# Optimization experiments

Measured on AMD Instinct MI355X. Metric: run time of the kernel, lower is better.

The kernel has to match this reference:

```python
import jax, jax.numpy as jnp
import numpy as np

S = 16384   # sequence length (tree derivation steps)
H = 512     # hidden size
E = 512     # action embedding size
R = 2048    # num_of_rules
L = 2       # GRU layers
PAD = -1    # learning_utils.PADDING_ACTION
OFF = 1     # learning_utils.UNIVERSAL_ACTION_OFFSET


def setup_inputs() -> dict:
    key = jax.random.key(0)
    ks = jax.random.split(key, 16)
    def n(k, shape, scale=0.05):
        return jax.random.normal(k, shape, jnp.float32) * scale
    emb = n(ks[1], (R + OFF, E)).at[PAD + OFF].set(0.0)  # padding_idx row zeroed
    return {
        "initial_state": n(ks[0], (L, 1, H)),
        "embedding": emb,
        "W_ih0": n(ks[2], (3 * H, 2 * E)),
        "W_hh0": n(ks[3], (3 * H, H)),
        "b_ih0": n(ks[4], (3 * H,)),
        "b_hh0": n(ks[5], (3 * H,)),
        "W_ih1": n(ks[6], (3 * H, H)),
        "W_hh1": n(ks[7], (3 * H, H)),
        "b_ih1": n(ks[8], (3 * H,)),
        "b_hh1": n(ks[9], (3 * H,)),
        "action_W": n(ks[10], (R, H)),
        "action_b": n(ks[11], (R,)),
        "value_W": n(ks[12], (1, H)),
        "value_b": n(ks[13], (1,)),
        "old_actions": jax.random.randint(ks[14], (S,), 0, R, jnp.int32),
        "old_parent_actions": jax.random.randint(ks[15], (S,), 0, R, jnp.int32),
    }


def gru_layer(x, h0, W_ih, W_hh, b_ih, b_hh):
    """Torch-semantics GRU over x:[S,In] with batch=1 squeezed; h0:[H]."""
    xi = x @ W_ih.T + b_ih  # precompute input gates [S, 3H]
    def step(h, xi_t):
        gh = h @ W_hh.T + b_hh
        xr, xz, xn = jnp.split(xi_t, 3)
        hr, hz, hn = jnp.split(gh, 3)
        r = jax.nn.sigmoid(xr + hr)
        z = jax.nn.sigmoid(xz + hz)
        nl = jnp.tanh(xn + r * hn)
        h_new = (1.0 - z) * nl + z * h
        return h_new, h_new
    _, out = jax.lax.scan(step, h0, xi)
    return out  # [S, H]


def reference(initial_state, embedding, W_ih0, W_hh0, b_ih0, b_hh0,
              W_ih1, W_hh1, b_ih1, b_hh1, action_W, action_b,
              value_W, value_b, old_actions, old_parent_actions):
    # teacher-forced shift: prepend PADDING_ACTION, drop last
    shifted = jnp.concatenate([jnp.array([PAD], old_actions.dtype), old_actions[:-1]])
    a_emb = embedding[shifted + OFF]             # [S, E]
    p_emb = embedding[old_parent_actions + OFF]  # [S, E]
    x = jnp.concatenate([a_emb, p_emb], axis=-1) # [S, 2E]
    h = gru_layer(x, initial_state[0, 0], W_ih0, W_hh0, b_ih0, b_hh0)
    out = gru_layer(h, initial_state[1, 0], W_ih1, W_hh1, b_ih1, b_hh1)
    log_probs = jax.nn.log_softmax(out @ action_W.T + action_b, axis=-1)  # [S, R]
    values = (out @ value_W.T + value_b)[:, 0]                            # [S]
    return log_probs, values
```

## Files before the change

kernel.cpp:

```cpp
#include <hip/hip_runtime.h>
#include <hip/hip_bf16.h>
#include <hip/hip_fp16.h>

typedef _Float16 f16;
typedef _Float16 f16x2 __attribute__((ext_vector_type(2)));
typedef _Float16 f16x4 __attribute__((ext_vector_type(4)));
typedef _Float16 f16x8 __attribute__((ext_vector_type(8)));
typedef float f32x4 __attribute__((ext_vector_type(4)));
typedef unsigned long long u64;

#define S_LEN 16384
#define NRULES 2048
#define CAP 2000000
#define FAST_TRIES 64

#define H1SEQ_OFF 0u
#define ACTW_OFF  (16u*1024*1024)
#define WIH0_OFF  (18u*1024*1024)
#define HB0F_OFF  (21u*1024*1024)
#define HB0S_OFF  (21u*1024*1024 + 4096)
#define HB1F_OFF  (21u*1024*1024 + 8192)
#define HB1S_OFF  (21u*1024*1024 + 12288)

#if __has_builtin(__builtin_amdgcn_rcpf)
#define RCPF(x) __builtin_amdgcn_rcpf(x)
#else
#define RCPF(x) (1.0f/(x))
#endif

union F2U { f16x2 f; unsigned u; };

__device__ __forceinline__ float sigf(float x){ return RCPF(1.0f + __expf(-x)); }
__device__ __forceinline__ float tanh_fast(float x){
  float ax = fabsf(x);
  float e = __expf(-2.0f*ax);
  float t = (1.0f - e) * RCPF(1.0f + e);
  return x >= 0.0f ? t : -t;
}
__device__ __forceinline__ float dot2(f16x2 a, f16x2 b, float c){
#if __has_builtin(__builtin_amdgcn_fdot2)
  return __builtin_amdgcn_fdot2(a, b, c, false);
#else
  return c + (float)a.x*(float)b.x + (float)a.y*(float)b.y;
#endif
}
__device__ __forceinline__ u64 aload64(const u64* p){
  return __hip_atomic_load(p, __ATOMIC_RELAXED, __HIP_MEMORY_SCOPE_AGENT);
}
__device__ __forceinline__ void apub64(u64* p, u64 v){
  (void)__hip_atomic_exchange(p, v, __ATOMIC_RELAXED, __HIP_MEMORY_SCOPE_AGENT);
}
__device__ __forceinline__ u64 load_sc0_u64(const u64* p){
  u64 v;
  asm volatile("global_load_dwordx2 %0, %1, off sc0\n\ts_waitcnt vmcnt(0)"
               : "=v"(v) : "v"(p) : "memory");
  return v;
}
__device__ __forceinline__ void store_u64(u64* p, u64 v){
  asm volatile("global_store_dwordx2 %0, %1, off"
               :: "v"(p), "v"(v) : "memory");
}

__global__ __launch_bounds__(256) void gather_x(
    const float* __restrict__ emb, const int* __restrict__ act,
    const int* __restrict__ par, f16* __restrict__ X)
{
  const int t = blockIdx.x, lid = threadIdx.x;
  const int ia = (t == 0) ? 0 : (act[t-1] + 1);
  const int ip = par[t] + 1;
  const int half = lid >> 7;
  const int k = (lid & 127) << 2;
  const float* src = emb + (size_t)(half ? ip : ia) * 512 + k;
  float4 v = *(const float4*)src;
  f16x4 o; o.x=(f16)v.x; o.y=(f16)v.y; o.z=(f16)v.z; o.w=(f16)v.w;
  *(f16x4*)&X[(size_t)t*1024 + (half<<9) + k] = o;
}

__global__ __launch_bounds__(256) void cvt_k(const float* __restrict__ in,
                                             f16* __restrict__ out, int n)
{
  const int i = (blockIdx.x*256 + threadIdx.x) << 2;
  if (i >= n) return;
  float4 v = *(const float4*)&in[i];
  f16x4 o; o.x=(f16)v.x; o.y=(f16)v.y; o.z=(f16)v.z; o.w=(f16)v.w;
  *(f16x4*)&out[i] = o;
}

__global__ __launch_bounds__(256) void init_ctrl(const float* __restrict__ init, char* ws)
{
  const int lid = threadIdx.x;
  u64* f0 = (u64*)(ws + HB0F_OFF);
  u64* s0 = (u64*)(ws + HB0S_OFF);
  u64* f1 = (u64*)(ws + HB1F_OFF);
  u64* s1 = (u64*)(ws + HB1S_OFF);
  F2U a; a.f.x=(f16)init[2*lid];     a.f.y=(f16)init[2*lid+1];
  F2U c; c.f.x=(f16)init[512+2*lid]; c.f.y=(f16)init[512+2*lid+1];
  const u64 inval = (u64)0xF0000000u << 32;
  const u64 sa = (u64)a.u, sc = (u64)c.u;
  f0[lid] = inval; f0[256+lid] = sa;
  s0[lid] = inval; s0[256+lid] = sa;
  f1[lid] = inval; f1[256+lid] = sc;
  s1[lid] = inval; s1[256+lid] = sc;
}

template<typename OutT>
__global__ __launch_bounds__(256) void gemm_f16(
    const f16* __restrict__ A, const f16* __restrict__ B,
    const float* __restrict__ bias, OutT* __restrict__ C,
    int M, int N, int K)
{
  __shared__ __align__(16) f16 At[4][128][8];
  __shared__ __align__(16) f16 Bt[4][128][8];
  const int lid = threadIdx.x;
  const int mtiles = M >> 7;
  const int bm = blockIdx.x % mtiles;
  const int bn = blockIdx.x / mtiles;
  const int m0 = bm << 7, n0 = bn << 7;
  const int lane = lid & 63, w = lid >> 6;
  const int wm = (w >> 1) << 6, wn = (w & 1) << 6;
  f32x4 acc[4][4] = {};
  const int nk = K >> 5;
  const int row1 = lid >> 2, j1 = lid & 3;
  for (int kt = 0; kt < nk; ++kt){
    const int kb = kt << 5;
    *(f16x8*)&At[j1][row1][0]    = *(const f16x8*)&A[(size_t)(m0+row1)*K    + kb + j1*8];
    *(f16x8*)&At[j1][row1+64][0] = *(const f16x8*)&A[(size_t)(m0+row1+64)*K + kb + j1*8];
    *(f16x8*)&Bt[j1][row1][0]    = *(const f16x8*)&B[(size_t)(n0+row1)*K    + kb + j1*8];
    *(f16x8*)&Bt[j1][row1+64][0] = *(const f16x8*)&B[(size_t)(n0+row1+64)*K + kb + j1*8];
    __syncthreads();
    const int kc = lane >> 4, rr = lane & 15;
    f16x8 aF[4], bF[4];
    #pragma unroll
    for (int m=0;m<4;m++) aF[m] = *(const f16x8*)&At[kc][wm + m*16 + rr][0];
    #pragma unroll
    for (int n=0;n<4;n++) bF[n] = *(const f16x8*)&Bt[kc][wn + n*16 + rr][0];
    #pragma unroll
    for (int m=0;m<4;m++)
      #pragma unroll
      for (int n=0;n<4;n++)
        acc[m][n] = __builtin_amdgcn_mfma_f32_16x16x32_f16(aF[m], bF[n], acc[m][n], 0,0,0);
    __syncthreads();
  }
  const int rr = lane & 15, rg = lane >> 4;
  #pragma unroll
  for (int n=0;n<4;n++){
    const int gcol = n0 + wn + n*16 + rr;
    const float bv = bias[gcol];
    #pragma unroll
    for (int m=0;m<4;m++){
      #pragma unroll
      for (int r=0;r<4;r++){
        const int grow = m0 + wm + m*16 + rg*4 + r;
        C[(size_t)grow*N + gcol] = (OutT)(acc[m][n][r] + bv);
      }
    }
  }
}

__global__ __launch_bounds__(256, 1) void scan_rings(
    const float* __restrict__ Whh0, const float* __restrict__ bhh0,
    const float* __restrict__ Wih1, const float* __restrict__ bih1,
    const float* __restrict__ Whh1, const float* __restrict__ bhh1,
    const float* __restrict__ init, const f16* __restrict__ xi0,
    u64* __restrict__ h0seq, char* ws)
{
  const int lid = threadIdx.x;
  const int bid = blockIdx.x;
  f16x2* h1seq = (f16x2*)(ws + H1SEQ_OFF);
  u64* hb0f = (u64*)(ws + HB0F_OFF);
  u64* hb0s = (u64*)(ws + HB0S_OFF);
  u64* hb1f = (u64*)(ws + HB1F_OFF);
  u64* hb1s = (u64*)(ws + HB1S_OFF);
  __shared__ f16x2 hx[256];
  __shared__ f16x2 hh[256];

  const int lane7 = bid & 7, grp = bid >> 3;
  bool fast_ok = true;

  if (lane7 == 0 && grp < 8){
    const int b = grp;
    const int ksub = lid & 3, row = (b << 6) + (lid >> 2);
    const bool owner = (ksub == 0);
    f16x2 wr[64], wz[64], wn[64];
    #pragma unroll
    for (int i=0;i<64;i++){
      const int k0 = (ksub + (i<<2)) << 1;
      float2 a = *(const float2*)&Whh0[(size_t)row*512         + k0];
      float2 bb= *(const float2*)&Whh0[(size_t)(512+row)*512   + k0];
      float2 c = *(const float2*)&Whh0[(size_t)(1024+row)*512  + k0];
      wr[i].x=(f16)a.x;  wr[i].y=(f16)a.y;
      wz[i].x=(f16)bb.x; wz[i].y=(f16)bb.y;
      wn[i].x=(f16)c.x;  wn[i].y=(f16)c.y;
    }
    float bhr=0.f, bhz=0.f, bhn=0.f;
    if (owner){ bhr=bhh0[row]; bhz=bhh0[512+row]; bhn=bhh0[1024+row]; }

    for (int q=0; q<S_LEN; ++q){
      float xr=0.f, xz=0.f, xn=0.f;
      if (owner){
        const f16* xp = xi0 + (size_t)q*1536;
        xr=(float)xp[row]; xz=(float)xp[512+row]; xn=(float)xp[1024+row];
      }
      {
        const int par = (q+1)&1;
        const u64* pf = hb0f + par*256 + lid;
        const u64* ps = hb0s + par*256 + lid;
        u64 cell = 0; bool got = false;
        if (fast_ok){
          for (int k=0;k<FAST_TRIES;k++){
            u64 v = load_sc0_u64(pf);
            if ((unsigned)(v>>32) == (unsigned)q){ cell=v; got=true; break; }
          }
          if (!got) fast_ok = false;
        }
        if (!got){
          int it=0;
          for(;;){ u64 v = aload64(ps);
                   if ((unsigned)(v>>32) == (unsigned)q){ cell=v; break; }
                   if (++it > CAP){ cell=v; break; } }
        }
        F2U cu; cu.u = (unsigned)cell; hx[lid] = cu.f;
      }
      __syncthreads();
      float ar=0.f, az=0.f, an=0.f;
      #pragma unroll
      for (int i=0;i<64;i++){
        f16x2 hv = hx[ksub + (i<<2)];
        ar = dot2(wr[i], hv, ar); az = dot2(wz[i], hv, az); an = dot2(wn[i], hv, an);
      }
      ar += __shfl_xor(ar,1); ar += __shfl_xor(ar,2);
      az += __shfl_xor(az,1); az += __shfl_xor(az,2);
      an += __shfl_xor(an,1); an += __shfl_xor(an,2);
      float hnew = 0.f;
      if (owner){
        float r  = sigf(xr + ar + bhr);
        float z  = sigf(xz + az + bhz);
        float nl = tanh_fast(xn + r*(an + bhn));
        hnew = (1.0f - z)*nl + z*(float)hx[row>>1][row&1];
      }
      float hp = __shfl(hnew, (lid & 192) + ((lid+4) & 63));
      if ((lid & 7) == 0){
        F2U pr; pr.f.x=(f16)hnew; pr.f.y=(f16)hp;
        const int j = (b<<5) + (lid>>3);
        const u64 tagged = ((u64)(unsigned)(q+1)<<32) | (u64)pr.u;
        store_u64(&hb0f[(q&1)*256 + j], tagged);
        apub64(&hb0s[(q&1)*256 + j], tagged);
        apub64(&h0seq[(size_t)q*256 + j], tagged);
      }
      __syncthreads();
    }
  } else if (lane7 == 1 && grp < 16){
    const int u = grp;
    const int ksub = lid & 7, row = (u << 5) + (lid >> 3);
    const bool owner = (ksub == 0);
    f16x2 ur[32], uz[32], un[32], vr[32], vz[32], vn[32];
    #pragma unroll
    for (int i=0;i<32;i++){
      const int k0 = (ksub + (i<<3)) << 1;
      float2 a = *(const float2*)&Wih1[(size_t)row*512        + k0];
      float2 bb= *(const float2*)&Wih1[(size_t)(512+row)*512  + k0];
      float2 c = *(const float2*)&Wih1[(size_t)(1024+row)*512 + k0];
      float2 d = *(const float2*)&Whh1[(size_t)row*512        + k0];
      float2 e = *(const float2*)&Whh1[(size_t)(512+row)*512  + k0];
      float2 f = *(const float2*)&Whh1[(size_t)(1024+row)*512 + k0];
      ur[i].x=(f16)a.x;  ur[i].y=(f16)a.y;
      uz[i].x=(f16)bb.x; uz[i].y=(f16)bb.y;
      un[i].x=(f16)c.x;  un[i].y=(f16)c.y;
      vr[i].x=(f16)d.x;  vr[i].y=(f16)d.y;
      vz[i].x=(f16)e.x;  vz[i].y=(f16)e.y;
      vn[i].x=(f16)f.x;  vn[i].y=(f16)f.y;
    }
    float bir=0.f,biz=0.f,bin=0.f, bhr=0.f,bhz=0.f,bhn=0.f;
    if (owner){
      bir=bih1[row]; biz=bih1[512+row]; bin=bih1[1024+row];
      bhr=bhh1[row]; bhz=bhh1[512+row]; bhn=bhh1[1024+row];
    }

    u64 ca_pref = 0;
    for (int t=0; t<S_LEN; ++t){
      const u64* pa = h0seq + (size_t)t*256 + lid;
      const int par = (t+1)&1;
      const u64* pf = hb1f + par*256 + lid;
      const u64* ps = hb1s + par*256 + lid;
      u64 ca=0, cb=0; bool ga=false, gb=false;
      if ((unsigned)(ca_pref>>32) == (unsigned)(t+1)){ ca=ca_pref; ga=true; }
      if (fast_ok){
        for (int k=0; k<FAST_TRIES && !(ga&&gb); ++k){
          if(!ga){ u64 v=aload64(pa);
                   if((unsigned)(v>>32)==(unsigned)(t+1)){ca=v;ga=true;} }
          if(!gb){ u64 v=load_sc0_u64(pf);
                   if((unsigned)(v>>32)==(unsigned)t){cb=v;gb=true;} }
        }
        if (!gb) fast_ok = false;
      }
      if (!(ga&&gb)){
        int it=0;
        while(!(ga&&gb)){
          if(!ga){ u64 v=aload64(pa);
                   if((unsigned)(v>>32)==(unsigned)(t+1)){ca=v;ga=true;} }
          if(!gb){ u64 v=aload64(ps);
                   if((unsigned)(v>>32)==(unsigned)t){cb=v;gb=true;} }
          if (++it > CAP) break;
        }
      }
      F2U xa; xa.u = (unsigned)ca; hx[lid] = xa.f;
      F2U hc; hc.u = (unsigned)cb; hh[lid] = hc.f;
      __syncthreads();
      if (t+1 < S_LEN) ca_pref = aload64(pa + 256);
      float ir=0.f, iz=0.f, in_=0.f, hr=0.f, hz=0.f, hn=0.f;
      #pragma unroll
      for (int i=0;i<32;i++){
        f16x2 xv = hx[ksub + (i<<3)];
        f16x2 hv = hh[ksub + (i<<3)];
        ir = dot2(ur[i], xv, ir); iz = dot2(uz[i], xv, iz); in_ = dot2(un[i], xv, in_);
        hr = dot2(vr[i], hv, hr); hz = dot2(vz[i], hv, hz); hn  = dot2(vn[i], hv, hn);
      }
      #pragma unroll
      for (int d=1; d<8; d<<=1){
        ir += __shfl_xor(ir,d); iz += __shfl_xor(iz,d); in_ += __shfl_xor(in_,d);
        hr += __shfl_xor(hr,d); hz += __shfl_xor(hz,d); hn  += __shfl_xor(hn,d);
      }
      float hnew = 0.f;
      if (owner){
        float r  = sigf(ir + bir + hr + bhr);
        float z  = sigf(iz + biz + hz + bhz);
        float nl = tanh_fast(in_ + bin + r*(hn + bhn));
        hnew = (1.0f - z)*nl + z*(float)hh[row>>1][row&1];
      }
      float hp = __shfl(hnew, (lid & 192) + ((lid+8) & 63));
      if ((lid & 15) == 0){
        F2U pr; pr.f.x=(f16)hnew; pr.f.y=(f16)hp;
        const int j = (u<<4) + (lid>>4);
        const u64 tagged = ((u64)(unsigned)(t+1)<<32) | (u64)pr.u;
        store_u64(&hb1f[(t&1)*256 + j], tagged);
        apub64(&hb1s[(t&1)*256 + j], tagged);
        h1seq[(size_t)t*256 + j] = pr.f;
      }
      __syncthreads();
    }
  }
}

__global__ __launch_bounds__(256) void logsoftmax_k(float* __restrict__ lp)
{
  const int t = blockIdx.x, lid = threadIdx.x;
  float* row = lp + (size_t)t*2048;
  float4 a = ((const float4*)row)[lid*2];
  float4 b = ((const float4*)row)[lid*2+1];
  float m = fmaxf(fmaxf(fmaxf(a.x,a.y),fmaxf(a.z,a.w)),
                  fmaxf(fmaxf(b.x,b.y),fmaxf(b.z,b.w)));
  #pragma unroll
  for (int off=1; off<64; off<<=1) m = fmaxf(m, __shfl_xor(m, off));
  __shared__ float redm[4], reds[4];
  const int lane = lid & 63, wvi = lid >> 6;
  if (lane==0) redm[wvi] = m;
  __syncthreads();
  m = fmaxf(fmaxf(redm[0],redm[1]), fmaxf(redm[2],redm[3]));
  float s = __expf(a.x-m)+__expf(a.y-m)+__expf(a.z-m)+__expf(a.w-m)
          + __expf(b.x-m)+__expf(b.y-m)+__expf(b.z-m)+__expf(b.w-m);
  #pragma unroll
  for (int off=1; off<64; off<<=1) s += __shfl_xor(s, off);
  if (lane==0) reds[wvi] = s;
  __syncthreads();
  s = reds[0]+reds[1]+reds[2]+reds[3];
  const float lg = m + __logf(s);
  a.x-=lg; a.y-=lg; a.z-=lg; a.w-=lg;
  b.x-=lg; b.y-=lg; b.z-=lg; b.w-=lg;
  ((float4*)row)[lid*2]   = a;
  ((float4*)row)[lid*2+1] = b;
}

__global__ __launch_bounds__(256) void values_k(
    const f16* __restrict__ h1, const float* __restrict__ vW,
    const float* __restrict__ vb, float* __restrict__ outv, int S)
{
  const int gt = (int)((blockIdx.x*256 + threadIdx.x) >> 6);
  if (gt >= S) return;
  const int lane = threadIdx.x & 63;
  const f16* rowp = h1 + (size_t)gt*512;
  float s = 0.f;
  #pragma unroll
  for (int j=0;j<8;j++){
    const int k = lane + (j<<6);
    s += (float)rowp[k] * vW[k];
  }
  #pragma unroll
  for (int off=32; off; off>>=1) s += __shfl_down(s, off);
  if (lane==0) outv[gt] = s + vb[0];
}

extern "C" void kernel_launch(void* const* d_in, const int* in_sizes, int n_in,
                              void* d_out, int out_size, void* d_ws, size_t ws_size,
                              hipStream_t stream) {
  const float* init = (const float*)d_in[0];
  const float* emb  = (const float*)d_in[1];
  const float* Wih0 = (const float*)d_in[2];
  const float* Whh0 = (const float*)d_in[3];
  const float* bih0 = (const float*)d_in[4];
  const float* bhh0 = (const float*)d_in[5];
  const float* Wih1 = (const float*)d_in[6];
  const float* Whh1 = (const float*)d_in[7];
  const float* bih1 = (const float*)d_in[8];
  const float* bhh1 = (const float*)d_in[9];
  const float* actW = (const float*)d_in[10];
  const float* actb = (const float*)d_in[11];
  const float* valW = (const float*)d_in[12];
  const float* valb = (const float*)d_in[13];
  const int*   acts = (const int*)d_in[14];
  const int*   pars = (const int*)d_in[15];
  float* out = (float*)d_out;
  char*  w   = (char*)d_ws;

  f16* h1seq = (f16*)(w + H1SEQ_OFF);
  f16* actWh = (f16*)(w + ACTW_OFF);
  f16* Wih0h = (f16*)(w + WIH0_OFF);
  f16* xi0   = (f16*)d_out;
  f16* X     = (f16*)((char*)d_out + 48u*1024*1024);
  u64* h0seq = (u64*)((char*)d_out + 80u*1024*1024);

  hipMemsetAsync(h0seq, 0, (size_t)S_LEN*256*8, stream);
  gather_x<<<S_LEN, 256, 0, stream>>>(emb, acts, pars, X);
  cvt_k<<<1536, 256, 0, stream>>>(Wih0, Wih0h, 1536*1024);
  cvt_k<<<1024, 256, 0, stream>>>(actW, actWh, 2048*512);
  init_ctrl<<<1, 256, 0, stream>>>(init, w);

  gemm_f16<f16><<<128*12, 256, 0, stream>>>(X, Wih0h, bih0, xi0, S_LEN, 1536, 1024);

  scan_rings<<<128, 256, 0, stream>>>(Whh0, bhh0, Wih1, bih1, Whh1, bhh1,
                                      init, xi0, h0seq, w);

  gemm_f16<float><<<128*16, 256, 0, stream>>>(h1seq, actWh, actb, out, S_LEN, NRULES, 512);
  logsoftmax_k<<<S_LEN, 256, 0, stream>>>(out);
  values_k<<<S_LEN/4, 256, 0, stream>>>(h1seq, valW, valb, out + (size_t)S_LEN*NRULES, S_LEN);
}
```

Before: 30.43 ms.

## Add dedicated publisher wavefront to scan blocks, decoupling global stores from compute waves

Each scan block gets a fifth wavefront that takes over publishing the new hidden state to the global ring buffers and sequence arrays. Compute waves now write hnew into shared memory and meet the publisher at lightweight barriers that wait only on LDS counters, which replaces the cross-lane shuffle pairing. The goal is to take global store and atomic latency off the compute waves' per-step critical path. The cost is one more wave per block and an extra shared-memory hop, and publication can still become a serialisation point.

Result: slower. 31.65 ms (+4.0%).

```diff
diff --git a/kernel.cpp b/kernel.cpp
--- a/kernel.cpp
+++ b/kernel.cpp
@@ -60,6 +60,7 @@
   asm volatile("global_store_dwordx2 %0, %1, off"
                :: "v"(p), "v"(v) : "memory");
 }
+#define BAR_LGKM() asm volatile("s_waitcnt lgkmcnt(0)\n\ts_barrier" ::: "memory")
 
 __global__ __launch_bounds__(256) void gather_x(
     const float* __restrict__ emb, const int* __restrict__ act,
@@ -157,7 +158,7 @@
   }
 }
 
-__global__ __launch_bounds__(256, 1) void scan_rings(
+__global__ __launch_bounds__(320, 1) void scan_rings(
     const float* __restrict__ Whh0, const float* __restrict__ bhh0,
     const float* __restrict__ Wih1, const float* __restrict__ bih1,
     const float* __restrict__ Whh1, const float* __restrict__ bhh1,
@@ -173,170 +174,184 @@
   u64* hb1s = (u64*)(ws + HB1S_OFF);
   __shared__ f16x2 hx[256];
   __shared__ f16x2 hh[256];
+  __shared__ float hnb[64];
 
   const int lane7 = bid & 7, grp = bid >> 3;
   bool fast_ok = true;
 
   if (lane7 == 0 && grp < 8){
     const int b = grp;
-    const int ksub = lid & 3, row = (b << 6) + (lid >> 2);
-    const bool owner = (ksub == 0);
-    f16x2 wr[64], wz[64], wn[64];
-    #pragma unroll
-    for (int i=0;i<64;i++){
-      const int k0 = (ksub + (i<<2)) << 1;
-      float2 a = *(const float2*)&Whh0[(size_t)row*512         + k0];
-      float2 bb= *(const float2*)&Whh0[(size_t)(512+row)*512   + k0];
-      float2 c = *(const float2*)&Whh0[(size_t)(1024+row)*512  + k0];
-      wr[i].x=(f16)a.x;  wr[i].y=(f16)a.y;
-      wz[i].x=(f16)bb.x; wz[i].y=(f16)bb.y;
-      wn[i].x=(f16)c.x;  wn[i].y=(f16)c.y;
-    }
-    float bhr=0.f, bhz=0.f, bhn=0.f;
-    if (owner){ bhr=bhh0[row]; bhz=bhh0[512+row]; bhn=bhh0[1024+row]; }
-
-    for (int q=0; q<S_LEN; ++q){
-      float xr=0.f, xz=0.f, xn=0.f;
-      if (owner){
-        const f16* xp = xi0 + (size_t)q*1536;
-        xr=(float)xp[row]; xz=(float)xp[512+row]; xn=(float)xp[1024+row];
-      }
-      {
-        const int par = (q+1)&1;
-        const u64* pf = hb0f + par*256 + lid;
-        const u64* ps = hb0s + par*256 + lid;
-        u64 cell = 0; bool got = false;
-        if (fast_ok){
-          for (int k=0;k<FAST_TRIES;k++){
-            u64 v = load_sc0_u64(pf);
-            if ((unsigned)(v>>32) == (unsigned)q){ cell=v; got=true; break; }
-          }
-          if (!got) fast_ok = false;
-        }
-        if (!got){
-          int it=0;
-          for(;;){ u64 v = aload64(ps);
-                   if ((unsigned)(v>>32) == (unsigned)q){ cell=v; break; }
-                   if (++it > CAP){ cell=v; break; } }
-        }
-        F2U cu; cu.u = (unsigned)cell; hx[lid] = cu.f;
-      }
-      __syncthreads();
-      float ar=0.f, az=0.f, an=0.f;
+    if (lid < 256){
+      const int ksub = lid & 3, row = (b << 6) + (lid >> 2);
+      const bool owner = (ksub == 0);
+      f16x2 wr[64], wz[64], wn[64];
       #pragma unroll
       for (int i=0;i<64;i++){
-        f16x2 hv = hx[ksub + (i<<2)];
-        ar = dot2(wr[i], hv, ar); az = dot2(wz[i], hv, az); an = dot2(wn[i], hv, an);
-      }
-      ar += __shfl_xor(ar,1); ar += __shfl_xor(ar,2);
-      az += __shfl_xor(az,1); az += __shfl_xor(az,2);
-      an += __shfl_xor(an,1); an += __shfl_xor(an,2);
-      float hnew = 0.f;
-      if (owner){
-        float r  = sigf(xr + ar + bhr);
-        float z  = sigf(xz + az + bhz);
-        float nl = tanh_fast(xn + r*(an + bhn));
-        hnew = (1.0f - z)*nl + z*(float)hx[row>>1][row&1];
-      }
-      float hp = __shfl(hnew, (lid & 192) + ((lid+4) & 63));
-      if ((lid & 7) == 0){
-        F2U pr; pr.f.x=(f16)hnew; pr.f.y=(f16)hp;
-        const int j = (b<<5) + (lid>>3);
-        const u64 tagged = ((u64)(unsigned)(q+1)<<32) | (u64)pr.u;
-        store_u64(&hb0f[(q&1)*256 + j], tagged);
-        apub64(&hb0s[(q&1)*256 + j], tagged);
-        apub64(&h0seq[(size_t)q*256 + j], tagged);
-      }
-      __syncthreads();
+        const int k0 = (ksub + (i<<2)) << 1;
+        float2 a = *(const float2*)&Whh0[(size_t)row*512         + k0];
+        float2 bb= *(const float2*)&Whh0[(size_t)(512+row)*512   + k0];
+        float2 c = *(const float2*)&Whh0[(size_t)(1024+row)*512  + k0];
+        wr[i].x=(f16)a.x;  wr[i].y=(f16)a.y;
+        wz[i].x=(f16)bb.x; wz[i].y=(f16)bb.y;
+        wn[i].x=(f16)c.x;  wn[i].y=(f16)c.y;
+      }
+      float bhr=0.f, bhz=0.f, bhn=0.f;
+      if (owner){ bhr=bhh0[row]; bhz=bhh0[512+row]; bhn=bhh0[1024+row]; }
+
+      for (int q=0; q<S_LEN; ++q){
+        float xr=0.f, xz=0.f, xn=0.f;
+        if (owner){
+          const f16* xp = xi0 + (size_t)q*1536;
+          xr=(float)xp[row]; xz=(float)xp[512+row]; xn=(float)xp[1024+row];
+        }
+        {
+          const int par = (q+1)&1;
+          const u64* pf = hb0f + par*256 + lid;
+          const u64* ps = hb0s + par*256 + lid;
+          u64 cell = 0; bool got = false;
+          if (fast_ok){
+            for (int k=0;k<FAST_TRIES;k++){
+              u64 v = load_sc0_u64(pf);
+              if ((unsigned)(v>>32) == (unsigned)q){ cell=v; got=true; break; }
+            }
+            if (!got) fast_ok = false;
+          }
+          if (!got){
+            int it=0;
+            for(;;){ u64 v = aload64(ps);
+                     if ((unsigned)(v>>32) == (unsigned)q){ cell=v; break; }
+                     if (++it > CAP){ cell=v; break; } }
+          }
+          F2U cu; cu.u = (unsigned)cell; hx[lid] = cu.f;
+        }
+        BAR_LGKM();
+        float ar=0.f, az=0.f, an=0.f;
+        #pragma unroll
+        for (int i=0;i<64;i++){
+          f16x2 hv = hx[ksub + (i<<2)];
+          ar = dot2(wr[i], hv, ar); az = dot2(wz[i], hv, az); an = dot2(wn[i], hv, an);
+        }
+        ar += __shfl_xor(ar,1); ar += __shfl_xor(ar,2);
+        az += __shfl_xor(az,1); az += __shfl_xor(az,2);
+        an += __shfl_xor(an,1); an += __shfl_xor(an,2);
+        if (owner){
+          float r  = sigf(xr + ar + bhr);
+          float z  = sigf(xz + az + bhz);
+          float nl = tanh_fast(xn + r*(an + bhn));
+          float hnew = (1.0f - z)*nl + z*(float)hx[row>>1][row&1];
+          hnb[lid>>2] = hnew;
+        }
+        BAR_LGKM();
+      }
+    } else {
+      const int pl = lid - 256;
+      for (int q=0; q<S_LEN; ++q){
+        BAR_LGKM();
+        BAR_LGKM();
+        if (pl < 32){
+          F2U pr; pr.f.x=(f16)hnb[2*pl]; pr.f.y=(f16)hnb[2*pl+1];
+          const int j = (b<<5) + pl;
+          const u64 tagged = ((u64)(unsigned)(q+1)<<32) | (u64)pr.u;
+          store_u64(&hb0f[(q&1)*256 + j], tagged);
+          apub64(&hb0s[(q&1)*256 + j], tagged);
+          apub64(&h0seq[(size_t)q*256 + j], tagged);
+        }
+      }
     }
   } else if (lane7 == 1 && grp < 16){
     const int u = grp;
-    const int ksub = lid & 7, row = (u << 5) + (lid >> 3);
-    const bool owner = (ksub == 0);
-    f16x2 ur[32], uz[32], un[32], vr[32], vz[32], vn[32];
-    #pragma unroll
-    for (int i=0;i<32;i++){
-      const int k0 = (ksub + (i<<3)) << 1;
-      float2 a = *(const float2*)&Wih1[(size_t)row*512        + k0];
-      float2 bb= *(const float2*)&Wih1[(size_t)(512+row)*512  + k0];
-      float2 c = *(const float2*)&Wih1[(size_t)(1024+row)*512 + k0];
-      float2 d = *(const float2*)&Whh1[(size_t)row*512        + k0];
-      float2 e = *(const float2*)&Whh1[(size_t)(512+row)*512  + k0];
-      float2 f = *(const float2*)&Whh1[(size_t)(1024+row)*512 + k0];
-      ur[i].x=(f16)a.x;  ur[i].y=(f16)a.y;
-      uz[i].x=(f16)bb.x; uz[i].y=(f16)bb.y;
-      un[i].x=(f16)c.x;  un[i].y=(f16)c.y;
-      vr[i].x=(f16)d.x;  vr[i].y=(f16)d.y;
-      vz[i].x=(f16)e.x;  vz[i].y=(f16)e.y;
-      vn[i].x=(f16)f.x;  vn[i].y=(f16)f.y;
-    }
-    float bir=0.f,biz=0.f,bin=0.f, bhr=0.f,bhz=0.f,bhn=0.f;
-    if (owner){
-      bir=bih1[row]; biz=bih1[512+row]; bin=bih1[1024+row];
-      bhr=bhh1[row]; bhz=bhh1[512+row]; bhn=bhh1[1024+row];
-    }
-
-    u64 ca_pref = 0;
-    for (int t=0; t<S_LEN; ++t){
-      const u64* pa = h0seq + (size_t)t*256 + lid;
-      const int par = (t+1)&1;
-      const u64* pf = hb1f + par*256 + lid;
-      const u64* ps = hb1s + par*256 + lid;
-      u64 ca=0, cb=0; bool ga=false, gb=false;
-      if ((unsigned)(ca_pref>>32) == (unsigned)(t+1)){ ca=ca_pref; ga=true; }
-      if (fast_ok){
-        for (int k=0; k<FAST_TRIES && !(ga&&gb); ++k){
-          if(!ga){ u64 v=aload64(pa);
-                   if((unsigned)(v>>32)==(unsigned)(t+1)){ca=v;ga=true;} }
-          if(!gb){ u64 v=load_sc0_u64(pf);
-                   if((unsigned)(v>>32)==(unsigned)t){cb=v;gb=true;} }
-        }
-        if (!gb) fast_ok = false;
-      }
-      if (!(ga&&gb)){
-        int it=0;
-        while(!(ga&&gb)){
-          if(!ga){ u64 v=aload64(pa);
-                   if((unsigned)(v>>32)==(unsigned)(t+1)){ca=v;ga=true;} }
-          if(!gb){ u64 v=aload64(ps);
-                   if((unsigned)(v>>32)==(unsigned)t){cb=v;gb=true;} }
-          if (++it > CAP) break;
-        }
-      }
-      F2U xa; xa.u = (unsigned)ca; hx[lid] = xa.f;
-      F2U hc; hc.u = (unsigned)cb; hh[lid] = hc.f;
-      __syncthreads();
-      if (t+1 < S_LEN) ca_pref = aload64(pa + 256);
-      float ir=0.f, iz=0.f, in_=0.f, hr=0.f, hz=0.f, hn=0.f;
+    if (lid < 256){
+      const int ksub = lid & 7, row = (u << 5) + (lid >> 3);
+      const bool owner = (ksub == 0);
+      f16x2 ur[32], uz[32], un[32], vr[32], vz[32], vn[32];
       #pragma unroll
       for (int i=0;i<32;i++){
-        f16x2 xv = hx[ksub + (i<<3)];
-        f16x2 hv = hh[ksub + (i<<3)];
-        ir = dot2(ur[i], xv, ir); iz = dot2(uz[i], xv, iz); in_ = dot2(un[i], xv, in_);
-        hr = dot2(vr[i], hv, hr); hz = dot2(vz[i], hv, hz); hn  = dot2(vn[i], hv, hn);
-      }
-      #pragma unroll
-      for (int d=1; d<8; d<<=1){
-        ir += __shfl_xor(ir,d); iz += __shfl_xor(iz,d); in_ += __shfl_xor(in_,d);
-        hr += __shfl_xor(hr,d); hz += __shfl_xor(hz,d); hn  += __shfl_xor(hn,d);
-      }
-      float hnew = 0.f;
+        const int k0 = (ksub + (i<<3)) << 1;
+        float2 a = *(const float2*)&Wih1[(size_t)row*512        + k0];
+        float2 bb= *(const float2*)&Wih1[(size_t)(512+row)*512  + k0];
+        float2 c = *(const float2*)&Wih1[(size_t)(1024+row)*512 + k0];
+        float2 d = *(const float2*)&Whh1[(size_t)row*512        + k0];
+        float2 e = *(const float2*)&Whh1[(size_t)(512+row)*512  + k0];
+        float2 f = *(const float2*)&Whh1[(size_t)(1024+row)*512 + k0];
+        ur[i].x=(f16)a.x;  ur[i].y=(f16)a.y;
+        uz[i].x=(f16)bb.x; uz[i].y=(f16)bb.y;
+        un[i].x=(f16)c.x;  un[i].y=(f16)c.y;
+        vr[i].x=(f16)d.x;  vr[i].y=(f16)d.y;
+        vz[i].x=(f16)e.x;  vz[i].y=(f16)e.y;
+        vn[i].x=(f16)f.x;  vn[i].y=(f16)f.y;
+      }
+      float bir=0.f,biz=0.f,bin=0.f, bhr=0.f,bhz=0.f,bhn=0.f;
       if (owner){
-        float r  = sigf(ir + bir + hr + bhr);
-        float z  = sigf(iz + biz + hz + bhz);
-        float nl = tanh_fast(in_ + bin + r*(hn + bhn));
-        hnew = (1.0f - z)*nl + z*(float)hh[row>>1][row&1];
-      }
-      float hp = __shfl(hnew, (lid & 192) + ((lid+8) & 63));
-      if ((lid & 15) == 0){
-        F2U pr; pr.f.x=(f16)hnew; pr.f.y=(f16)hp;
-        const int j = (u<<4) + (lid>>4);
-        const u64 tagged = ((u64)(unsigned)(t+1)<<32) | (u64)pr.u;
-        store_u64(&hb1f[(t&1)*256 + j], tagged);
-        apub64(&hb1s[(t&1)*256 + j], tagged);
-        h1seq[(size_t)t*256 + j] = pr.f;
-      }
-      __syncthreads();
+        bir=bih1[row]; biz=bih1[512+row]; bin=bih1[1024+row];
+        bhr=bhh1[row]; bhz=bhh1[512+row]; bhn=bhh1[1024+row];
+      }
+
+      for (int t=0; t<S_LEN; ++t){
+        {
+          const u64* pa = h0seq + (size_t)t*256 + lid;
+          const int par = (t+1)&1;
+          const u64* pf = hb1f + par*256 + lid;
+          const u64* ps = hb1s + par*256 + lid;
+          u64 ca=0, cb=0; bool ga=false, gb=false;
+          if (fast_ok){
+            for (int k=0; k<FAST_TRIES && !(ga&&gb); ++k){
+              if(!ga){ u64 v=aload64(pa);
+                       if((unsigned)(v>>32)==(unsigned)(t+1)){ca=v;ga=true;} }
+              if(!gb){ u64 v=load_sc0_u64(pf);
+                       if((unsigned)(v>>32)==(unsigned)t){cb=v;gb=true;} }
+            }
+            if (!gb) fast_ok = false;
+          }
+          if (!(ga&&gb)){
+            int it=0;
+            while(!(ga&&gb)){
+              if(!ga){ u64 v=aload64(pa);
+                       if((unsigned)(v>>32)==(unsigned)(t+1)){ca=v;ga=true;} }
+              if(!gb){ u64 v=aload64(ps);
+                       if((unsigned)(v>>32)==(unsigned)t){cb=v;gb=true;} }
+              if (++it > CAP) break;
+            }
+          }
+          F2U xa; xa.u = (unsigned)ca; hx[lid] = xa.f;
+          F2U hc; hc.u = (unsigned)cb; hh[lid] = hc.f;
+        }
+        BAR_LGKM();
+        float ir=0.f, iz=0.f, in_=0.f, hr=0.f, hz=0.f, hn=0.f;
+        #pragma unroll
+        for (int i=0;i<32;i++){
+          f16x2 xv = hx[ksub + (i<<3)];
+          f16x2 hv = hh[ksub + (i<<3)];
+          ir = dot2(ur[i], xv, ir); iz = dot2(uz[i], xv, iz); in_ = dot2(un[i], xv, in_);
+          hr = dot2(vr[i], hv, hr); hz = dot2(vz[i], hv, hz); hn  = dot2(vn[i], hv, hn);
+        }
+        #pragma unroll
+        for (int d=1; d<8; d<<=1){
+          ir += __shfl_xor(ir,d); iz += __shfl_xor(iz,d); in_ += __shfl_xor(in_,d);
+          hr += __shfl_xor(hr,d); hz += __shfl_xor(hz,d); hn  += __shfl_xor(hn,d);
+        }
+        if (owner){
+          float r  = sigf(ir + bir + hr + bhr);
+          float z  = sigf(iz + biz + hz + bhz);
+          float nl = tanh_fast(in_ + bin + r*(hn + bhn));
+          float hnew = (1.0f - z)*nl + z*(float)hh[row>>1][row&1];
+          hnb[lid>>3] = hnew;
+        }
+        BAR_LGKM();
+      }
+    } else {
+      const int pl = lid - 256;
+      for (int t=0; t<S_LEN; ++t){
+        BAR_LGKM();
+        BAR_LGKM();
+        if (pl < 16){
+          F2U pr; pr.f.x=(f16)hnb[2*pl]; pr.f.y=(f16)hnb[2*pl+1];
+          const int j = (u<<4) + pl;
+          const u64 tagged = ((u64)(unsigned)(t+1)<<32) | (u64)pr.u;
+          store_u64(&hb1f[(t&1)*256 + j], tagged);
+          apub64(&hb1s[(t&1)*256 + j], tagged);
+          h1seq[(size_t)t*256 + j] = pr.f;
+        }
+      }
     }
   }
 }
@@ -426,7 +441,7 @@
 
   gemm_f16<f16><<<128*12, 256, 0, stream>>>(X, Wih0h, bih0, xi0, S_LEN, 1536, 1024);
 
-  scan_rings<<<128, 256, 0, stream>>>(Whh0, bhh0, Wih1, bih1, Whh1, bhh1,
+  scan_rings<<<128, 320, 0, stream>>>(Whh0, bhh0, Wih1, bih1, Whh1, bhh1,
                                       init, xi0, h0seq, w);
 
   gemm_f16<float><<<128*16, 256, 0, stream>>>(h1seq, actWh, actb, out, S_LEN, NRULES, 512);
```

## Co-locate both GRU layers per workgroup and pass layer-0 state through shared memory

Applied to the files above, without the earlier changes.

Replaces the separate layer-0 and layer-1 ring workgroups with 16 workgroups of 768 threads. Each one holds a 32-row slice of layer 0 and a 32-row slice of layer 1, with layer 1 running one step behind layer 0 inside the same loop. Layer-0 output reaches layer 1 through LDS instead of a global h0seq buffer, and cross-workgroup exchange still goes through tagged flag rings. This removes the h0seq memset, the global staging and polling between layers, and prefetches the next step's input gates. The cost is spreading layer-0 rows over 16 blocks instead of 8, which means more participants in each cross-block sync. Barriers now use s_waitcnt lgkmcnt plus s_barrier.

New measurement: 53.70 ms. 1.76x slower.

```diff
diff --git a/kernel.cpp b/kernel.cpp
--- a/kernel.cpp
+++ b/kernel.cpp
@@ -60,6 +60,7 @@
   asm volatile("global_store_dwordx2 %0, %1, off"
                :: "v"(p), "v"(v) : "memory");
 }
+#define BAR_LGKM() asm volatile("s_waitcnt lgkmcnt(0)\n\ts_barrier" ::: "memory")
 
 __global__ __launch_bounds__(256) void gather_x(
     const float* __restrict__ emb, const int* __restrict__ act,
@@ -86,21 +87,18 @@
   *(f16x4*)&out[i] = o;
 }
 
-__global__ __launch_bounds__(256) void init_ctrl(const float* __restrict__ init, char* ws)
+__global__ __launch_bounds__(256) void init_ctrl(char* ws)
 {
   const int lid = threadIdx.x;
-  u64* f0 = (u64*)(ws + HB0F_OFF);
-  u64* s0 = (u64*)(ws + HB0S_OFF);
-  u64* f1 = (u64*)(ws + HB1F_OFF);
-  u64* s1 = (u64*)(ws + HB1S_OFF);
-  F2U a; a.f.x=(f16)init[2*lid];     a.f.y=(f16)init[2*lid+1];
-  F2U c; c.f.x=(f16)init[512+2*lid]; c.f.y=(f16)init[512+2*lid+1];
   const u64 inval = (u64)0xF0000000u << 32;
-  const u64 sa = (u64)a.u, sc = (u64)c.u;
-  f0[lid] = inval; f0[256+lid] = sa;
-  s0[lid] = inval; s0[256+lid] = sa;
-  f1[lid] = inval; f1[256+lid] = sc;
-  s1[lid] = inval; s1[256+lid] = sc;
+  u64* F0 = (u64*)(ws + HB0F_OFF);
+  u64* S0 = (u64*)(ws + HB0S_OFF);
+  u64* F1 = (u64*)(ws + HB1F_OFF);
+  u64* S1 = (u64*)(ws + HB1S_OFF);
+  F0[lid]=inval; F0[256+lid]=inval;
+  S0[lid]=inval; S0[256+lid]=inval;
+  F1[lid]=inval; F1[256+lid]=inval;
+  S1[lid]=inval; S1[256+lid]=inval;
 }
 
 template<typename OutT>
@@ -157,186 +155,186 @@
   }
 }
 
-__global__ __launch_bounds__(256, 1) void scan_rings(
+__global__ __launch_bounds__(768, 1) void scan_m(
     const float* __restrict__ Whh0, const float* __restrict__ bhh0,
     const float* __restrict__ Wih1, const float* __restrict__ bih1,
     const float* __restrict__ Whh1, const float* __restrict__ bhh1,
     const float* __restrict__ init, const f16* __restrict__ xi0,
-    u64* __restrict__ h0seq, char* ws)
-{
-  const int lid = threadIdx.x;
-  const int bid = blockIdx.x;
+    char* ws)
+{
+  const int lid = threadIdx.x, bid = blockIdx.x;
+  if (bid & 7) return;
+  const int grp = bid >> 3;
   f16x2* h1seq = (f16x2*)(ws + H1SEQ_OFF);
-  u64* hb0f = (u64*)(ws + HB0F_OFF);
-  u64* hb0s = (u64*)(ws + HB0S_OFF);
-  u64* hb1f = (u64*)(ws + HB1F_OFF);
-  u64* hb1s = (u64*)(ws + HB1S_OFF);
-  __shared__ f16x2 hx[256];
-  __shared__ f16x2 hh[256];
-
-  const int lane7 = bid & 7, grp = bid >> 3;
+  u64* F0 = (u64*)(ws + HB0F_OFF);
+  u64* S0 = (u64*)(ws + HB0S_OFF);
+  u64* F1 = (u64*)(ws + HB1F_OFF);
+  u64* S1 = (u64*)(ws + HB1S_OFF);
+  __shared__ f16x2 hb[2][512];
   bool fast_ok = true;
 
-  if (lane7 == 0 && grp < 8){
-    const int b = grp;
-    const int ksub = lid & 3, row = (b << 6) + (lid >> 2);
+  if (lid < 256){
+    const int ksub = lid & 7, r = lid >> 3, row = (grp << 5) + r;
     const bool owner = (ksub == 0);
-    f16x2 wr[64], wz[64], wn[64];
-    #pragma unroll
-    for (int i=0;i<64;i++){
-      const int k0 = (ksub + (i<<2)) << 1;
-      float2 a = *(const float2*)&Whh0[(size_t)row*512         + k0];
-      float2 bb= *(const float2*)&Whh0[(size_t)(512+row)*512   + k0];
-      float2 c = *(const float2*)&Whh0[(size_t)(1024+row)*512  + k0];
-      wr[i].x=(f16)a.x;  wr[i].y=(f16)a.y;
-      wz[i].x=(f16)bb.x; wz[i].y=(f16)bb.y;
-      wn[i].x=(f16)c.x;  wn[i].y=(f16)c.y;
-    }
-    float bhr=0.f, bhz=0.f, bhn=0.f;
-    if (owner){ bhr=bhh0[row]; bhz=bhh0[512+row]; bhn=bhh0[1024+row]; }
-
-    for (int q=0; q<S_LEN; ++q){
-      float xr=0.f, xz=0.f, xn=0.f;
-      if (owner){
-        const f16* xp = xi0 + (size_t)q*1536;
-        xr=(float)xp[row]; xz=(float)xp[512+row]; xn=(float)xp[1024+row];
-      }
-      {
-        const int par = (q+1)&1;
-        const u64* pf = hb0f + par*256 + lid;
-        const u64* ps = hb0s + par*256 + lid;
-        u64 cell = 0; bool got = false;
-        if (fast_ok){
-          for (int k=0;k<FAST_TRIES;k++){
-            u64 v = load_sc0_u64(pf);
-            if ((unsigned)(v>>32) == (unsigned)q){ cell=v; got=true; break; }
-          }
-          if (!got) fast_ok = false;
-        }
-        if (!got){
-          int it=0;
-          for(;;){ u64 v = aload64(ps);
-                   if ((unsigned)(v>>32) == (unsigned)q){ cell=v; break; }
-                   if (++it > CAP){ cell=v; break; } }
-        }
-        F2U cu; cu.u = (unsigned)cell; hx[lid] = cu.f;
-      }
-      __syncthreads();
-      float ar=0.f, az=0.f, an=0.f;
-      #pragma unroll
-      for (int i=0;i<64;i++){
-        f16x2 hv = hx[ksub + (i<<2)];
-        ar = dot2(wr[i], hv, ar); az = dot2(wz[i], hv, az); an = dot2(wn[i], hv, an);
-      }
-      ar += __shfl_xor(ar,1); ar += __shfl_xor(ar,2);
-      az += __shfl_xor(az,1); az += __shfl_xor(az,2);
-      an += __shfl_xor(an,1); an += __shfl_xor(an,2);
-      float hnew = 0.f;
-      if (owner){
-        float r  = sigf(xr + ar + bhr);
-        float z  = sigf(xz + az + bhz);
-        float nl = tanh_fast(xn + r*(an + bhn));
-        hnew = (1.0f - z)*nl + z*(float)hx[row>>1][row&1];
-      }
-      float hp = __shfl(hnew, (lid & 192) + ((lid+4) & 63));
-      if ((lid & 7) == 0){
-        F2U pr; pr.f.x=(f16)hnew; pr.f.y=(f16)hp;
-        const int j = (b<<5) + (lid>>3);
-        const u64 tagged = ((u64)(unsigned)(q+1)<<32) | (u64)pr.u;
-        store_u64(&hb0f[(q&1)*256 + j], tagged);
-        apub64(&hb0s[(q&1)*256 + j], tagged);
-        apub64(&h0seq[(size_t)q*256 + j], tagged);
-      }
-      __syncthreads();
-    }
-  } else if (lane7 == 1 && grp < 16){
-    const int u = grp;
-    const int ksub = lid & 7, row = (u << 5) + (lid >> 3);
-    const bool owner = (ksub == 0);
-    f16x2 ur[32], uz[32], un[32], vr[32], vz[32], vn[32];
+    f16x2 wr[32], wz[32], wn[32];
     #pragma unroll
     for (int i=0;i<32;i++){
       const int k0 = (ksub + (i<<3)) << 1;
-      float2 a = *(const float2*)&Wih1[(size_t)row*512        + k0];
-      float2 bb= *(const float2*)&Wih1[(size_t)(512+row)*512  + k0];
-      float2 c = *(const float2*)&Wih1[(size_t)(1024+row)*512 + k0];
-      float2 d = *(const float2*)&Whh1[(size_t)row*512        + k0];
-      float2 e = *(const float2*)&Whh1[(size_t)(512+row)*512  + k0];
-      float2 f = *(const float2*)&Whh1[(size_t)(1024+row)*512 + k0];
-      ur[i].x=(f16)a.x;  ur[i].y=(f16)a.y;
-      uz[i].x=(f16)bb.x; uz[i].y=(f16)bb.y;
-      un[i].x=(f16)c.x;  un[i].y=(f16)c.y;
-      vr[i].x=(f16)d.x;  vr[i].y=(f16)d.y;
-      vz[i].x=(f16)e.x;  vz[i].y=(f16)e.y;
-      vn[i].x=(f16)f.x;  vn[i].y=(f16)f.y;
+      float2 a = *(const float2*)&Whh0[(size_t)row*512         + k0];
+      float2 b = *(const float2*)&Whh0[(size_t)(512+row)*512   + k0];
+      float2 c = *(const float2*)&Whh0[(size_t)(1024+row)*512  + k0];
+      wr[i].x=(f16)a.x; wr[i].y=(f16)a.y;
+      wz[i].x=(f16)b.x; wz[i].y=(f16)b.y;
+      wn[i].x=(f16)c.x; wn[i].y=(f16)c.y;
+    }
+    float bhr=0.f,bhz=0.f,bhn=0.f, xr=0.f,xz=0.f,xn=0.f, pxr=0.f,pxz=0.f,pxn=0.f;
+    if (owner){
+      bhr=bhh0[row]; bhz=bhh0[512+row]; bhn=bhh0[1024+row];
+      xr=(float)xi0[row]; xz=(float)xi0[512+row]; xn=(float)xi0[1024+row];
+    }
+    { F2U s; s.f.x=(f16)init[2*lid]; s.f.y=(f16)init[2*lid+1]; hb[0][lid]=s.f; }
+    BAR_LGKM();
+
+    for (int q=0; q<=S_LEN; ++q){
+      const int p = (q+1)&1;
+      if (q < S_LEN){
+        if (owner && q+1 < S_LEN){
+          const f16* xp = xi0 + (size_t)(q+1)*1536;
+          pxr=(float)xp[row]; pxz=(float)xp[512+row]; pxn=(float)xp[1024+row];
+        }
+        const f16x2* cur = hb[q&1];
+        float ar=0.f, az=0.f, an=0.f;
+        #pragma unroll
+        for (int i=0;i<32;i++){
+          f16x2 hv = cur[ksub + (i<<3)];
+          ar = dot2(wr[i],hv,ar); az = dot2(wz[i],hv,az); an = dot2(wn[i],hv,an);
+        }
+        ar += __shfl_xor(ar,1); ar += __shfl_xor(ar,2); ar += __shfl_xor(ar,4);
+        az += __shfl_xor(az,1); az += __shfl_xor(az,2); az += __shfl_xor(az,4);
+        an += __shfl_xor(an,1); an += __shfl_xor(an,2); an += __shfl_xor(an,4);
+        float hnew = 0.f;
+        if (owner){
+          float r_ = sigf(xr + ar + bhr);
+          float z_ = sigf(xz + az + bhz);
+          float nl = tanh_fast(xn + r_*(an + bhn));
+          hnew = (1.0f - z_)*nl + z_*(float)cur[row>>1][row&1];
+          xr=pxr; xz=pxz; xn=pxn;
+        }
+        float hp = __shfl(hnew, ((lid&63)+8)&63);
+        if ((lid & 15) == 0){
+          F2U pr; pr.f.x=(f16)hnew; pr.f.y=(f16)hp;
+          const int j = (grp<<4) + (lid>>4);
+          const u64 tg = ((u64)(unsigned)(q+1)<<32) | (u64)pr.u;
+          store_u64(&F0[p*256 + j], tg);
+          apub64(&S0[p*256 + j], tg);
+        }
+        {
+          const u64* pf = F0 + p*256 + lid;
+          const u64* ps = S0 + p*256 + lid;
+          u64 cell=0; bool got=false;
+          if (fast_ok){
+            for (int k=0;k<FAST_TRIES;k++){
+              u64 v = load_sc0_u64(pf);
+              if ((unsigned)(v>>32) == (unsigned)(q+1)){ cell=v; got=true; break; }
+            }
+            if (!got) fast_ok = false;
+          }
+          if (!got){
+            int it=0;
+            for(;;){ u64 v = aload64(ps);
+                     if ((unsigned)(v>>32) == (unsigned)(q+1)){ cell=v; break; }
+                     if (++it > CAP){ cell=v; break; } }
+          }
+          F2U cu; cu.u = (unsigned)cell; hb[p][lid] = cu.f;
+        }
+      }
+      BAR_LGKM();
+    }
+  } else {
+    const int local = lid - 256;
+    const int ksub16 = local & 15, ksubh = ksub16 & 7;
+    const int r = local >> 4, row = (grp << 5) + r;
+    const bool grpA = (ksub16 < 8);
+    const bool owner = (ksub16 == 0);
+    const float* Wsel = grpA ? Wih1 : Whh1;
+    const int base = grpA ? 0 : 256;
+    f16x2 wa[32], wb[32], wc[32];
+    #pragma unroll
+    for (int i=0;i<32;i++){
+      const int k0 = (ksubh + (i<<3)) << 1;
+      float2 a = *(const float2*)&Wsel[(size_t)row*512         + k0];
+      float2 b = *(const float2*)&Wsel[(size_t)(512+row)*512   + k0];
+      float2 c = *(const float2*)&Wsel[(size_t)(1024+row)*512  + k0];
+      wa[i].x=(f16)a.x; wa[i].y=(f16)a.y;
+      wb[i].x=(f16)b.x; wb[i].y=(f16)b.y;
+      wc[i].x=(f16)c.x; wc[i].y=(f16)c.y;
     }
     float bir=0.f,biz=0.f,bin=0.f, bhr=0.f,bhz=0.f,bhn=0.f;
     if (owner){
       bir=bih1[row]; biz=bih1[512+row]; bin=bih1[1024+row];
       bhr=bhh1[row]; bhz=bhh1[512+row]; bhn=bhh1[1024+row];
     }
-
-    u64 ca_pref = 0;
-    for (int t=0; t<S_LEN; ++t){
-      const u64* pa = h0seq + (size_t)t*256 + lid;
-      const int par = (t+1)&1;
-      const u64* pf = hb1f + par*256 + lid;
-      const u64* ps = hb1s + par*256 + lid;
-      u64 ca=0, cb=0; bool ga=false, gb=false;
-      if ((unsigned)(ca_pref>>32) == (unsigned)(t+1)){ ca=ca_pref; ga=true; }
-      if (fast_ok){
-        for (int k=0; k<FAST_TRIES && !(ga&&gb); ++k){
-          if(!ga){ u64 v=aload64(pa);
-                   if((unsigned)(v>>32)==(unsigned)(t+1)){ca=v;ga=true;} }
-          if(!gb){ u64 v=load_sc0_u64(pf);
-                   if((unsigned)(v>>32)==(unsigned)t){cb=v;gb=true;} }
-        }
-        if (!gb) fast_ok = false;
+    if (local < 256){
+      F2U s; s.f.x=(f16)init[512+2*local]; s.f.y=(f16)init[512+2*local+1];
+      hb[0][256+local] = s.f;
+    }
+    BAR_LGKM();
+
+    for (int q=0; q<=S_LEN; ++q){
+      const int p = (q+1)&1;
+      if (q >= 1){
+        const f16x2* cur = hb[q&1];
+        float sa=0.f, sb=0.f, sc=0.f;
+        #pragma unroll
+        for (int i=0;i<32;i++){
+          f16x2 hv = cur[base + ksubh + (i<<3)];
+          sa = dot2(wa[i],hv,sa); sb = dot2(wb[i],hv,sb); sc = dot2(wc[i],hv,sc);
+        }
+        sa += __shfl_xor(sa,1); sa += __shfl_xor(sa,2); sa += __shfl_xor(sa,4);
+        sb += __shfl_xor(sb,1); sb += __shfl_xor(sb,2); sb += __shfl_xor(sb,4);
+        sc += __shfl_xor(sc,1); sc += __shfl_xor(sc,2); sc += __shfl_xor(sc,4);
+        float oa = __shfl_xor(sa,8), ob = __shfl_xor(sb,8), oc = __shfl_xor(sc,8);
+        float hnew = 0.f;
+        if (owner){
+          float r_ = sigf(sa + bir + oa + bhr);
+          float z_ = sigf(sb + biz + ob + bhz);
+          float nl = tanh_fast(sc + bin + r_*(oc + bhn));
+          hnew = (1.0f - z_)*nl + z_*(float)cur[256 + (row>>1)][row&1];
+        }
+        float hp = __shfl(hnew, ((lid&63)+16)&63);
+        if ((local & 31) == 0){
+          F2U pr; pr.f.x=(f16)hnew; pr.f.y=(f16)hp;
+          const int j = (grp<<4) + (local>>5);
+          h1seq[(size_t)(q-1)*256 + j] = pr.f;
+          if (q < S_LEN){
+            const u64 tg = ((u64)(unsigned)(q+1)<<32) | (u64)pr.u;
+            store_u64(&F1[p*256 + j], tg);
+            apub64(&S1[p*256 + j], tg);
+          }
+        }
       }
-      if (!(ga&&gb)){
-        int it=0;
-        while(!(ga&&gb)){
-          if(!ga){ u64 v=aload64(pa);
-                   if((unsigned)(v>>32)==(unsigned)(t+1)){ca=v;ga=true;} }
-          if(!gb){ u64 v=aload64(ps);
-                   if((unsigned)(v>>32)==(unsigned)t){cb=v;gb=true;} }
-          if (++it > CAP) break;
-        }
+      if (q == 0){
+        if (local < 256) hb[1][256+local] = hb[0][256+local];
+      } else if (q < S_LEN && local < 256){
+        const u64* pf = F1 + p*256 + local;
+        const u64* ps = S1 + p*256 + local;
+        u64 cell=0; bool got=false;
+        if (fast_ok){
+          for (int k=0;k<FAST_TRIES;k++){
+            u64 v = load_sc0_u64(pf);
+            if ((unsigned)(v>>32) == (unsigned)(q+1)){ cell=v; got=true; break; }
+          }
+          if (!got) fast_ok = false;
+        }
+        if (!got){
+          int it=0;
+          for(;;){ u64 v = aload64(ps);
+                   if ((unsigned)(v>>32) == (unsigned)(q+1)){ cell=v; break; }
+                   if (++it > CAP){ cell=v; break; } }
+        }
+        F2U cu; cu.u = (unsigned)cell; hb[p][256+local] = cu.f;
       }
-      F2U xa; xa.u = (unsigned)ca; hx[lid] = xa.f;
-      F2U hc; hc.u = (unsigned)cb; hh[lid] = hc.f;
-      __syncthreads();
-      if (t+1 < S_LEN) ca_pref = aload64(pa + 256);
-      float ir=0.f, iz=0.f, in_=0.f, hr=0.f, hz=0.f, hn=0.f;
-      #pragma unroll
-      for (int i=0;i<32;i++){
-        f16x2 xv = hx[ksub + (i<<3)];
-        f16x2 hv = hh[ksub + (i<<3)];
-        ir = dot2(ur[i], xv, ir); iz = dot2(uz[i], xv, iz); in_ = dot2(un[i], xv, in_);
-        hr = dot2(vr[i], hv, hr); hz = dot2(vz[i], hv, hz); hn  = dot2(vn[i], hv, hn);
-      }
-      #pragma unroll
-      for (int d=1; d<8; d<<=1){
-        ir += __shfl_xor(ir,d); iz += __shfl_xor(iz,d); in_ += __shfl_xor(in_,d);
-        hr += __shfl_xor(hr,d); hz += __shfl_xor(hz,d); hn  += __shfl_xor(hn,d);
-      }
-      float hnew = 0.f;
-      if (owner){
-        float r  = sigf(ir + bir + hr + bhr);
-        float z  = sigf(iz + biz + hz + bhz);
-        float nl = tanh_fast(in_ + bin + r*(hn + bhn));
-        hnew = (1.0f - z)*nl + z*(float)hh[row>>1][row&1];
-      }
-      float hp = __shfl(hnew, (lid & 192) + ((lid+8) & 63));
-      if ((lid & 15) == 0){
-        F2U pr; pr.f.x=(f16)hnew; pr.f.y=(f16)hp;
-        const int j = (u<<4) + (lid>>4);
-        const u64 tagged = ((u64)(unsigned)(t+1)<<32) | (u64)pr.u;
-        store_u64(&hb1f[(t&1)*256 + j], tagged);
-        apub64(&hb1s[(t&1)*256 + j], tagged);
-        h1seq[(size_t)t*256 + j] = pr.f;
-      }
-      __syncthreads();
+      BAR_LGKM();
     }
   }
 }
@@ -414,20 +412,18 @@
   f16* h1seq = (f16*)(w + H1SEQ_OFF);
   f16* actWh = (f16*)(w + ACTW_OFF);
   f16* Wih0h = (f16*)(w + WIH0_OFF);
-  f16* xi0   = (f16*)d_out;
-  f16* X     = (f16*)((char*)d_out + 48u*1024*1024);
-  u64* h0seq = (u64*)((char*)d_out + 80u*1024*1024);
-
-  hipMemsetAsync(h0seq, 0, (size_t)S_LEN*256*8, stream);
+  f16* xi0 = (f16*)d_out;
+  f16* X   = (f16*)((char*)d_out + 48u*1024*1024);
+
   gather_x<<<S_LEN, 256, 0, stream>>>(emb, acts, pars, X);
   cvt_k<<<1536, 256, 0, stream>>>(Wih0, Wih0h, 1536*1024);
   cvt_k<<<1024, 256, 0, stream>>>(actW, actWh, 2048*512);
-  init_ctrl<<<1, 256, 0, stream>>>(init, w);
+  init_ctrl<<<1, 256, 0, stream>>>(w);
 
   gemm_f16<f16><<<128*12, 256, 0, stream>>>(X, Wih0h, bih0, xi0, S_LEN, 1536, 1024);
 
-  scan_rings<<<128, 256, 0, stream>>>(Whh0, bhh0, Wih1, bih1, Whh1, bhh1,
-                                      init, xi0, h0seq, w);
+  scan_m<<<128, 768, 0, stream>>>(Whh0, bhh0, Wih1, bih1, Whh1, bhh1,
+                                  init, xi0, w);
 
   gemm_f16<float><<<128*16, 256, 0, stream>>>(h1seq, actWh, actb, out, S_LEN, NRULES, 512);
   logsoftmax_k<<<S_LEN, 256, 0, stream>>>(out);
```
